# Performance work log

Measured on AMD Instinct MI355X. Metric: run time of the kernel, lower is better.

Reference implementation:

```python
import jax, jax.numpy as jnp
import numpy as np

BN_EPS = 1e-5


def setup_inputs() -> dict:
    key = jax.random.key(0)
    ks = jax.random.split(key, 6)
    B, C, H, W = 4, 256, 64, 64
    Ci = 128
    s_in = 0.02  # small init scale for conv weights
    x = jax.random.normal(ks[0], (B, C, H, W), dtype=jnp.float32)
    g_w = jax.random.normal(ks[1], (Ci, C), dtype=jnp.float32) * s_in
    theta_w = jax.random.normal(ks[2], (Ci, C), dtype=jnp.float32) * s_in
    phi_w = jax.random.normal(ks[3], (Ci, C), dtype=jnp.float32) * s_in
    W_w = jax.random.normal(ks[4], (C, Ci), dtype=jnp.float32) * s_in
    return {
        "x": x,
        "g_w": g_w, "g_b": jnp.zeros((Ci,), jnp.float32),
        "theta_w": theta_w, "theta_b": jnp.zeros((Ci,), jnp.float32),
        "phi_w": phi_w, "phi_b": jnp.zeros((Ci,), jnp.float32),
        "W_w": W_w, "W_b": jnp.zeros((C,), jnp.float32),
        "bn_gamma": jnp.ones((C,), jnp.float32),
        "bn_beta": jnp.zeros((C,), jnp.float32),
    }


def reference(x, g_w, g_b, theta_w, theta_b, phi_w, phi_b, W_w, W_b, bn_gamma, bn_beta):
    B, C, H, W = x.shape
    N = H * W
    xf = x.reshape(B, C, N)  # flatten spatial -> [B, C, N]

    def conv1x1(w, b):  # 1x1 conv == per-position linear over channels
        return jnp.einsum('oc,bcn->bon', w, xf) + b[None, :, None]

    g_x = conv1x1(g_w, g_b)          # [B, Ci, N]
    theta_x = conv1x1(theta_w, theta_b)
    phi_x = conv1x1(phi_w, phi_b)

    f = jnp.einsum('bcn,bcm->bnm', theta_x, phi_x)   # [B, N, N] attention logits
    attn = jax.nn.softmax(f, axis=-1)
    y = jnp.einsum('bnm,bcm->bcn', attn, g_x)        # [B, Ci, N]

    Wy = jnp.einsum('oc,bcn->bon', W_w, y) + W_b[None, :, None]  # [B, C, N]
    Wy = Wy.reshape(B, C, H, W)

    # BatchNorm2d in training mode (default): batch statistics over (B, H, W)
    mean = Wy.mean(axis=(0, 2, 3))
    var = Wy.var(axis=(0, 2, 3))
    Wy_bn = (bn_gamma[None, :, None, None] * (Wy - mean[None, :, None, None])
             * jax.lax.rsqrt(var[None, :, None, None] + BN_EPS)
             + bn_beta[None, :, None, None])
    return Wy_bn + x
```

## Files before the change

kernel.cpp:

```cpp
#include <hip/hip_runtime.h>
#include <hip/hip_bf16.h>

typedef __attribute__((ext_vector_type(8))) __bf16 bf16x8;
typedef __attribute__((ext_vector_type(4))) __bf16 bf16x4;
typedef __attribute__((ext_vector_type(4))) float  f32x4;
typedef __attribute__((ext_vector_type(16))) float f32x16;

#define L2E 1.44269504088896340736f

static __device__ __forceinline__ f32x4 mfma16(bf16x8 a, bf16x8 b, f32x4 c) {
    return __builtin_amdgcn_mfma_f32_16x16x32_bf16(a, b, c, 0, 0, 0);
}
static __device__ __forceinline__ f32x16 mfma32(bf16x8 a, bf16x8 b, f32x16 c) {
    return __builtin_amdgcn_mfma_f32_32x32x16_bf16(a, b, c, 0, 0, 0);
}

#define GLOAD_LDS16(gsrc, ldst)                                                \
    __builtin_amdgcn_global_load_lds(                                          \
        (const __attribute__((address_space(1))) unsigned int*)(gsrc),         \
        (__attribute__((address_space(3))) unsigned int*)(ldst), 16, 0, 0)

__global__ __launch_bounds__(256) void prep_w(
    const float* __restrict__ thw, const float* __restrict__ phw,
    const float* __restrict__ gw,  const float* __restrict__ Ww,
    __bf16* __restrict__ wbf)
{
    const int idx  = blockIdx.x * 256 + threadIdx.x;
    const int base = idx * 4;
    const float* src = (base < 32768) ? thw : (base < 65536) ? phw
                     : (base < 98304) ? gw  : Ww;
    const int off = base & 32767;
    f32x4 v = *reinterpret_cast<const f32x4*>(src + off);
    bf16x4 o;
    #pragma unroll
    for (int i = 0; i < 4; ++i) o[i] = (__bf16)v[i];
    *reinterpret_cast<bf16x4*>(wbf + base) = o;
}

__global__ __launch_bounds__(256) void xT_kernel(
    const float* __restrict__ x, __bf16* __restrict__ xT)
{
    __shared__ float tile[64][65];
    const int b  = blockIdx.z;
    const int c0 = blockIdx.y * 64;
    const int n0 = blockIdx.x * 64;
    const int tr = threadIdx.x >> 4;
    const int tc = threadIdx.x & 15;
    #pragma unroll
    for (int k = 0; k < 4; ++k) {
        int c = k * 16 + tr;
        f32x4 v = *reinterpret_cast<const f32x4*>(
            x + ((size_t)b * 256 + c0 + c) * 4096 + n0 + tc * 4);
        #pragma unroll
        for (int i = 0; i < 4; ++i) tile[c][tc * 4 + i] = v[i];
    }
    __syncthreads();
    #pragma unroll
    for (int k = 0; k < 4; ++k) {
        int n = k * 16 + tr;
        bf16x4 v;
        #pragma unroll
        for (int i = 0; i < 4; ++i) v[i] = (__bf16)tile[tc * 4 + i][n];
        *reinterpret_cast<bf16x4*>(xT + ((size_t)b * 4096 + n0 + n) * 256 + c0 + tc * 4) = v;
    }
}

__global__ __launch_bounds__(256, 1) void proj_mfma(
    const __bf16* __restrict__ xT, const __bf16* __restrict__ wbf,
    const float* __restrict__ bth, const float* __restrict__ bph,
    const float* __restrict__ bg,
    __bf16* __restrict__ thetaT, __bf16* __restrict__ phiT, __bf16* __restrict__ gT)
{
    const int p    = blockIdx.y;
    const int b    = blockIdx.z;
    const int n0   = blockIdx.x * 64;
    const int w    = threadIdx.x >> 6;
    const int lane = threadIdx.x & 63;
    const int lo   = lane & 15;
    const int hi   = lane >> 4;

    __shared__ alignas(16) __bf16 XA[64 * 256];
    __shared__ alignas(16) __bf16 WL[128 * 256];

    const __bf16* wsrc  = wbf + p * 32768;
    const float*  bias  = (p == 0) ? bth : (p == 1) ? bph : bg;
    __bf16*       out   = (p == 0) ? thetaT : (p == 1) ? phiT : gT;
    const __bf16* xbase = xT + ((size_t)b * 4096 + n0) * 256;

    #pragma unroll
    for (int u = 0; u < 8; ++u) {
        const int chunk = (w * 8 + u) * 64 + lane;
        const int row   = chunk >> 5;
        const int jb    = (chunk & 31) * 16;
        const int sb    = row * 512 + (jb ^ ((row & 7) << 4));
        GLOAD_LDS16(xbase + (sb >> 1), &XA[(w * 8 + u) * 512]);
    }
    #pragma unroll
    for (int u = 0; u < 16; ++u) {
        const int chunk = (w * 16 + u) * 64 + lane;
        const int row   = chunk >> 5;
        const int jb    = (chunk & 31) * 16;
        const int sb    = row * 512 + (jb ^ ((row & 7) << 4));
        GLOAD_LDS16(wsrc + (sb >> 1), &WL[(w * 16 + u) * 512]);
    }
    __syncthreads();

    f32x4 C[8];
    #pragma unroll
    for (int cc = 0; cc < 8; ++cc) C[cc] = f32x4{0.f, 0.f, 0.f, 0.f};

    const int arow = w * 16 + lo;
    #pragma unroll
    for (int kb = 0; kb < 8; ++kb) {
        const int koff = kb * 64 + hi * 16;
        bf16x8 a = *reinterpret_cast<const bf16x8*>(
            (const char*)XA + arow * 512 + (koff ^ ((arow & 7) << 4)));
        bf16x8 bb[8];
        #pragma unroll
        for (int cc = 0; cc < 8; ++cc) {
            const int o = cc * 16 + lo;
            bb[cc] = *reinterpret_cast<const bf16x8*>(
                (const char*)WL + o * 512 + (koff ^ ((o & 7) << 4)));
        }
        #pragma unroll
        for (int cc = 0; cc < 8; ++cc) C[cc] = mfma16(a, bb[cc], C[cc]);
    }

    const int nbase = n0 + w * 16;
    #pragma unroll
    for (int cc = 0; cc < 8; ++cc) {
        const float bv = bias[cc * 16 + lo];
        #pragma unroll
        for (int r = 0; r < 4; ++r)
            out[((size_t)b * 4096 + nbase + 4 * hi + r) * 128 + cc * 16 + lo] =
                (__bf16)(C[cc][r] + bv);
    }
}

__global__ __launch_bounds__(256) void transpose_g(
    const __bf16* __restrict__ gT, __bf16* __restrict__ gBlk)
{
    __shared__ __bf16 tile[64][66];
    const int b  = blockIdx.z;
    const int c0 = blockIdx.y * 64;
    const int n0 = blockIdx.x * 64;
    const int tr = threadIdx.x >> 4;
    const int tc = threadIdx.x & 15;
    #pragma unroll
    for (int k = 0; k < 4; ++k) {
        int row = k * 16 + tr;
        bf16x4 v = *reinterpret_cast<const bf16x4*>(
            gT + ((size_t)b * 4096 + n0 + row) * 128 + c0 + tc * 4);
        #pragma unroll
        for (int i = 0; i < 4; ++i) tile[row][tc * 4 + i] = v[i];
    }
    __syncthreads();
    #pragma unroll
    for (int k = 0; k < 4; ++k) {
        int c = k * 16 + tr;
        int n = n0 + tc * 4;
        int mt = n >> 5, mm = n & 31;
        int g  = mm >> 2;
        int gp = (g & 4) | ((g & 1) << 1) | ((g >> 1) & 1);
        int mmP = (gp << 2) | (mm & 3);
        bf16x4 v;
        #pragma unroll
        for (int i = 0; i < 4; ++i) v[i] = tile[tc * 4 + i][c];
        *reinterpret_cast<bf16x4*>(
            gBlk + (((size_t)(b * 128 + mt) * 128) + (c0 + c)) * 32 + mmP) = v;
    }
}

template<int NCH>
__global__ __launch_bounds__(256, 3) void attn_kernel(
    const __bf16* __restrict__ thetaT, const __bf16* __restrict__ phiT,
    const __bf16* __restrict__ gBlk, __bf16* __restrict__ yPart,
    float* __restrict__ lPart)
{
    constexpr int SH = (NCH == 8) ? 3 : 2;
    constexpr int NT = (4096 / NCH) / 32;
    const int bid   = blockIdx.x;
    const int chunk = bid & (NCH - 1);
    const int qb    = (bid >> SH) & 31;
    const int b     = bid >> (SH + 5);
    const int w     = threadIdx.x >> 6;
    const int lane  = threadIdx.x & 63;
    const int l31   = lane & 31;
    const int h2    = lane >> 5;
    const int Q0    = qb * 128 + w * 32;
    const int kvbase = chunk * (4096 / NCH);

    __shared__ alignas(16) __bf16 Kt[3][32 * 128];
    __shared__ alignas(16) __bf16 Vt[3][128 * 32];

    bf16x8 qf[8];
    {
        const __bf16* qrow = thetaT + ((size_t)b * 4096 + Q0 + l31) * 128 + h2 * 8;
        #pragma unroll
        for (int ks = 0; ks < 8; ++ks)
            qf[ks] = *reinterpret_cast<const bf16x8*>(qrow + ks * 16);
    }

    f32x16 yacc[4];
    #pragma unroll
    for (int ct = 0; ct < 4; ++ct)
        #pragma unroll
        for (int r = 0; r < 16; ++r) yacc[ct][r] = 0.f;
    float ylrun = 0.f;

    const __bf16* phiB   = phiT + (size_t)b * 4096 * 128;
    const __bf16* gBlk_b = gBlk + (size_t)b * 128 * 4096;

    auto stage = [&](int buf, int t) {
        const int kv = kvbase + t * 32;
        #pragma unroll
        for (int u = 0; u < 2; ++u) {
            const int ii   = w + u * 4;
            const int mrow = ii * 4 + (lane >> 4);
            const int cbl  = ((lane & 15) * 16) ^ ((mrow & 7) << 4);
            const __bf16* src = phiB + ((size_t)(kv + mrow) << 7) + (cbl >> 1);
            GLOAD_LDS16(src, &Kt[buf][ii * 512]);
        }
        const __bf16* vtile = gBlk_b + ((size_t)(kv >> 5) << 12);
        #pragma unroll
        for (int u = 0; u < 2; ++u) {
            const int jj = w + u * 4;
            const int ch = jj * 64 + lane;
            const int c  = ch >> 2;
            const int h  = (ch & 3) ^ ((c >> 1) & 3);
            const __bf16* src = vtile + c * 32 + h * 8;
            GLOAD_LDS16(src, &Vt[buf][jj * 512]);
        }
    };

    stage(0, 0);
    stage(1, 1);

    int ia = 0, ib = 1, ic = 2;
    const int sw = (l31 >> 1) & 3;

    #pragma unroll 1
    for (int t = 0; t < NT; ++t) {
        if (t < NT - 2) {
            stage(ic, t + 2);
            asm volatile("s_waitcnt vmcnt(8)" ::: "memory");
        } else if (t == NT - 2) {
            asm volatile("s_waitcnt vmcnt(4)" ::: "memory");
        } else {
            asm volatile("s_waitcnt vmcnt(0)" ::: "memory");
        }
        __builtin_amdgcn_s_barrier();
        __builtin_amdgcn_sched_barrier(0);

        const char* Kb = (const char*)&Kt[ia][0];
        const char* Vb = (const char*)&Vt[ia][0];

        f32x16 S;
        #pragma unroll
        for (int r = 0; r < 16; ++r) S[r] = 0.f;
        #pragma unroll
        for (int ks = 0; ks < 8; ++ks) {
            bf16x8 ka = *reinterpret_cast<const bf16x8*>(
                Kb + l31 * 256 + ((ks * 32 + h2 * 16) ^ ((l31 & 7) << 4)));
            S = mfma32(ka, qf[ks], S);
        }

        float p[16];
        #pragma unroll
        for (int r = 0; r < 16; ++r) p[r] = __builtin_amdgcn_exp2f(S[r] * L2E);
        float ls = 0.f;
        #pragma unroll
        for (int r = 0; r < 16; ++r) ls += p[r];
        ylrun += ls;
        bf16x8 pa0, pa1;
        #pragma unroll
        for (int e = 0; e < 8; ++e) { pa0[e] = (__bf16)p[e]; pa1[e] = (__bf16)p[8 + e]; }

        #pragma unroll
        for (int ct = 0; ct < 4; ++ct) {
            const int vrow = (ct * 32 + l31) * 64;
            bf16x8 v0 = *reinterpret_cast<const bf16x8*>(
                Vb + vrow + ((h2 ^ sw) << 4));
            bf16x8 v1 = *reinterpret_cast<const bf16x8*>(
                Vb + vrow + (((2 + h2) ^ sw) << 4));
            yacc[ct] = mfma32(pa0, v0, yacc[ct]);
            yacc[ct] = mfma32(pa1, v1, yacc[ct]);
        }

        asm volatile("" ::: "memory");
        __builtin_amdgcn_s_barrier();
        __builtin_amdgcn_sched_barrier(0);
        const int tmp = ia; ia = ib; ib = ic; ic = tmp;
    }

    const float ylt = ylrun + __shfl_xor(ylrun, 32);
    const int bc = chunk * 4 + b;
    #pragma unroll
    for (int ct = 0; ct < 4; ++ct)
        #pragma unroll
        for (int r = 0; r < 16; ++r) {
            const int q = Q0 + (r & 3) + 8 * (r >> 2) + 4 * h2;
            yPart[((size_t)bc * 4096 + q) * 128 + ct * 32 + l31] = (__bf16)yacc[ct][r];
        }
    if (h2 == 0)
        lPart[(size_t)bc * 4096 + Q0 + l31] = ylt;
}

template<int NC>
__global__ __launch_bounds__(256) void merge_kernel(
    const __bf16* __restrict__ yPart, const float* __restrict__ lPart,
    __bf16* __restrict__ yT)
{
    const int idx = blockIdx.x * 256 + threadIdx.x;
    const int row = idx >> 5;
    const int c4  = (idx & 31) * 4;
    float lsum = 0.f;
    #pragma unroll
    for (int c = 0; c < NC; ++c) lsum += lPart[(size_t)c * 16384 + row];
    const float inv = 1.0f / lsum;
    float s[4] = {0.f, 0.f, 0.f, 0.f};
    #pragma unroll
    for (int c = 0; c < NC; ++c) {
        bf16x4 v = *reinterpret_cast<const bf16x4*>(
            yPart + (size_t)c * 2097152 + (size_t)row * 128 + c4);
        #pragma unroll
        for (int i = 0; i < 4; ++i) s[i] += (float)v[i];
    }
    bf16x4 o;
    #pragma unroll
    for (int i = 0; i < 4; ++i) o[i] = (__bf16)(s[i] * inv);
    *reinterpret_cast<bf16x4*>(yT + (size_t)row * 128 + c4) = o;
}

__global__ __launch_bounds__(256, 1) void wy_mfma(
    const __bf16* __restrict__ yT, const __bf16* __restrict__ wW,
    const float* __restrict__ Wb, float* __restrict__ Wy, float* __restrict__ pSQ)
{
    const int b    = blockIdx.y;
    const int n0   = blockIdx.x * 128;
    const int w    = threadIdx.x >> 6;
    const int lane = threadIdx.x & 63;
    const int lo   = lane & 15;
    const int hi   = lane >> 4;

    __shared__ alignas(16) __bf16 YL[128 * 128];
    __shared__ alignas(16) __bf16 WL[256 * 128];

    const __bf16* ybase = yT + ((size_t)b * 4096 + n0) * 128;
    #pragma unroll
    for (int u = 0; u < 8; ++u) {
        const int chunk = (w * 8 + u) * 64 + lane;
        const int row   = chunk >> 4;
        const int jb    = (chunk & 15) * 16;
        const int sb    = row * 256 + (jb ^ ((row & 7) << 4));
        GLOAD_LDS16(ybase + (sb >> 1), &YL[(w * 8 + u) * 512]);
    }
    #pragma unroll
    for (int u = 0; u < 16; ++u) {
        const int chunk = (w * 16 + u) * 64 + lane;
        const int row   = chunk >> 4;
        const int jb    = (chunk & 15) * 16;
        const int sb    = row * 256 + (jb ^ ((row & 7) << 4));
        GLOAD_LDS16(wW + (sb >> 1), &WL[(w * 16 + u) * 512]);
    }
    __syncthreads();

    f32x4 C[4][8];
    #pragma unroll
    for (int og = 0; og < 4; ++og)
        #pragma unroll
        for (int ct = 0; ct < 8; ++ct) C[og][ct] = f32x4{0.f, 0.f, 0.f, 0.f};

    #pragma unroll
    for (int kb = 0; kb < 4; ++kb) {
        const int koff = kb * 64 + hi * 16;
        bf16x8 a[4], bb[8];
        #pragma unroll
        for (int og = 0; og < 4; ++og) {
            const int o = w * 64 + og * 16 + lo;
            a[og] = *reinterpret_cast<const bf16x8*>(
                (const char*)WL + o * 256 + (koff ^ ((o & 7) << 4)));
        }
        #pragma unroll
        for (int ct = 0; ct < 8; ++ct) {
            const int nl = ct * 16 + lo;
            bb[ct] = *reinterpret_cast<const bf16x8*>(
                (const char*)YL + nl * 256 + (koff ^ ((nl & 7) << 4)));
        }
        #pragma unroll
        for (int og = 0; og < 4; ++og)
            #pragma unroll
            for (int ct = 0; ct < 8; ++ct)
                C[og][ct] = mfma16(a[og], bb[ct], C[og][ct]);
    }

    const int blk = blockIdx.y * 32 + blockIdx.x;
    #pragma unroll
    for (int og = 0; og < 4; ++og)
        #pragma unroll
        for (int r = 0; r < 4; ++r) {
            const int o  = w * 64 + og * 16 + 4 * hi + r;
            const float bv = Wb[o];
            float s = 0.f, q = 0.f;
            #pragma unroll
            for (int ct = 0; ct < 8; ++ct) {
                const float v = C[og][ct][r] + bv;
                Wy[((size_t)b * 256 + o) * 4096 + n0 + ct * 16 + lo] = v;
                s += v; q += v * v;
            }
            #pragma unroll
            for (int off = 1; off <= 8; off <<= 1) {
                s += __shfl_xor(s, off);
                q += __shfl_xor(q, off);
            }
            if (lo == 0) {
                pSQ[blk * 256 + o]         = s;
                pSQ[32768 + blk * 256 + o] = q;
            }
        }
}

__global__ __launch_bounds__(128) void stats_finalize(
    const float* __restrict__ pSQ, const float* __restrict__ gamma,
    const float* __restrict__ beta, float* __restrict__ stats)
{
    const int o = blockIdx.x;
    const int t = threadIdx.x;
    float s = pSQ[t * 256 + o];
    float q = pSQ[32768 + t * 256 + o];
    #pragma unroll
    for (int off = 32; off >= 1; off >>= 1) {
        s += __shfl_down(s, off);
        q += __shfl_down(q, off);
    }
    __shared__ float red[4];
    if ((t & 63) == 0) { red[t >> 6] = s; red[2 + (t >> 6)] = q; }
    __syncthreads();
    if (t == 0) {
        const float S = red[0] + red[1];
        const float Q = red[2] + red[3];
        const float mean = S * (1.f / 16384.f);
        const float var  = Q * (1.f / 16384.f) - mean * mean;
        const float scl  = gamma[o] * rsqrtf(var + 1e-5f);
        stats[o]       = scl;
        stats[256 + o] = beta[o] - mean * scl;
    }
}

__global__ __launch_bounds__(256) void final_kernel(
    const float* __restrict__ Wy, const float* __restrict__ x,
    const float* __restrict__ stats, float* __restrict__ out)
{
    const int idx = blockIdx.x * 256 + threadIdx.x;
    const int o   = (idx >> 10) & 255;
    f32x4 wy = *reinterpret_cast<const f32x4*>(Wy + (size_t)idx * 4);
    f32x4 xv = *reinterpret_cast<const f32x4*>(x  + (size_t)idx * 4);
    f32x4 res = wy * stats[o] + stats[256 + o] + xv;
    *reinterpret_cast<f32x4*>(out + (size_t)idx * 4) = res;
}

extern "C" void kernel_launch(void* const* d_in, const int* in_sizes, int n_in,
                              void* d_out, int out_size, void* d_ws, size_t ws_size,
                              hipStream_t stream)
{
    const float* x    = (const float*)d_in[0];
    const float* g_w  = (const float*)d_in[1];
    const float* g_b  = (const float*)d_in[2];
    const float* th_w = (const float*)d_in[3];
    const float* th_b = (const float*)d_in[4];
    const float* ph_w = (const float*)d_in[5];
    const float* ph_b = (const float*)d_in[6];
    const float* W_w  = (const float*)d_in[7];
    const float* W_b  = (const float*)d_in[8];
    const float* bn_g = (const float*)d_in[9];
    const float* bn_b = (const float*)d_in[10];
    float* out = (float*)d_out;

    char* ws = (char*)d_ws;
    const size_t MB = 1u << 20;
    __bf16* thetaT = (__bf16*)(ws);
    __bf16* phiT   = (__bf16*)(ws + 4 * MB);
    __bf16* gBlk   = (__bf16*)(ws + 8 * MB);
    __bf16* gT     = (__bf16*)(ws + 12 * MB);
    __bf16* xT     = (__bf16*)(ws + 16 * MB);
    __bf16* yPart  = (__bf16*)(ws + 12 * MB);
    __bf16* yT     = (__bf16*)(ws);
    float*  Wy     = (float*) (ws + 4 * MB);
    float*  pSQ    = (float*) (ws + 20 * MB);

    const bool big = ws_size >= 46926848ull;
    const size_t tail = big ? 44 * MB : 28 * MB;
    float*  lPart = (float*) (ws + tail);
    __bf16* wbf   = (__bf16*)(ws + tail + (big ? 524288 : 262144));
    float*  stats = (float*) (ws + tail + (big ? 786432 : 524288));

    prep_w<<<dim3(128), 256, 0, stream>>>(th_w, ph_w, g_w, W_w, wbf);
    xT_kernel<<<dim3(64, 4, 4), 256, 0, stream>>>(x, xT);
    proj_mfma<<<dim3(64, 3, 4), 256, 0, stream>>>(
        xT, wbf, th_b, ph_b, g_b, thetaT, phiT, gT);
    transpose_g<<<dim3(64, 2, 4), 256, 0, stream>>>(gT, gBlk);
    if (big) {
        attn_kernel<8><<<dim3(1024), 256, 0, stream>>>(thetaT, phiT, gBlk, yPart, lPart);
        merge_kernel<8><<<dim3(2048), 256, 0, stream>>>(yPart, lPart, yT);
    } else {
        attn_kernel<4><<<dim3(512), 256, 0, stream>>>(thetaT, phiT, gBlk, yPart, lPart);
        merge_kernel<4><<<dim3(2048), 256, 0, stream>>>(yPart, lPart, yT);
    }
    wy_mfma<<<dim3(32, 4), 256, 0, stream>>>(yT, wbf + 98304, W_b, Wy, pSQ);
    stats_finalize<<<dim3(256), 128, 0, stream>>>(pSQ, bn_g, bn_b, stats);
    final_kernel<<<dim3(4096), 256, 0, stream>>>(Wy, x, stats, out);
}
```

Baseline: 102.1 us.

## Process two query tiles per wave in attention kernel with 2-wave blocks

Each wave now handles 64 query rows as two 32-row tiles and reuses every K and V fragment read from LDS for both tiles. The block shrinks from four waves to two, and each wave issues twice as many global-to-LDS loads per stage, with the vmcnt waits raised to match. The aim is to halve LDS read traffic per MFMA and raise arithmetic intensity. In exchange, per-wave register pressure roughly doubles (two sets of accumulators, Q fragments and S tiles), which may cut occupancy or cause spills, and there are fewer waves per block to hide latency.

Result: slower. 122.6 us (+20.1%).

```diff
diff --git a/kernel.cpp b/kernel.cpp
--- a/kernel.cpp
+++ b/kernel.cpp
@@ -172,7 +172,7 @@
 }
 
 template<int NCH>
-__global__ __launch_bounds__(256, 3) void attn_kernel(
+__global__ __launch_bounds__(128) void attn_kernel(
     const __bf16* __restrict__ thetaT, const __bf16* __restrict__ phiT,
     const __bf16* __restrict__ gBlk, __bf16* __restrict__ yPart,
     float* __restrict__ lPart)
@@ -187,26 +187,29 @@
     const int lane  = threadIdx.x & 63;
     const int l31   = lane & 31;
     const int h2    = lane >> 5;
-    const int Q0    = qb * 128 + w * 32;
+    const int Q0    = qb * 128 + w * 64;
     const int kvbase = chunk * (4096 / NCH);
 
     __shared__ alignas(16) __bf16 Kt[3][32 * 128];
     __shared__ alignas(16) __bf16 Vt[3][128 * 32];
 
-    bf16x8 qf[8];
-    {
-        const __bf16* qrow = thetaT + ((size_t)b * 4096 + Q0 + l31) * 128 + h2 * 8;
+    bf16x8 qf[2][8];
+    #pragma unroll
+    for (int j = 0; j < 2; ++j) {
+        const __bf16* qrow = thetaT + ((size_t)b * 4096 + Q0 + j * 32 + l31) * 128 + h2 * 8;
         #pragma unroll
         for (int ks = 0; ks < 8; ++ks)
-            qf[ks] = *reinterpret_cast<const bf16x8*>(qrow + ks * 16);
-    }
-
-    f32x16 yacc[4];
-    #pragma unroll
-    for (int ct = 0; ct < 4; ++ct)
-        #pragma unroll
-        for (int r = 0; r < 16; ++r) yacc[ct][r] = 0.f;
-    float ylrun = 0.f;
+            qf[j][ks] = *reinterpret_cast<const bf16x8*>(qrow + ks * 16);
+    }
+
+    f32x16 yacc[2][4];
+    #pragma unroll
+    for (int j = 0; j < 2; ++j)
+        #pragma unroll
+        for (int ct = 0; ct < 4; ++ct)
+            #pragma unroll
+            for (int r = 0; r < 16; ++r) yacc[j][ct][r] = 0.f;
+    float ylrun0 = 0.f, ylrun1 = 0.f;
 
     const __bf16* phiB   = phiT + (size_t)b * 4096 * 128;
     const __bf16* gBlk_b = gBlk + (size_t)b * 128 * 4096;
@@ -214,22 +217,22 @@
     auto stage = [&](int buf, int t) {
         const int kv = kvbase + t * 32;
         #pragma unroll
-        for (int u = 0; u < 2; ++u) {
-            const int ii   = w + u * 4;
-            const int mrow = ii * 4 + (lane >> 4);
-            const int cbl  = ((lane & 15) * 16) ^ ((mrow & 7) << 4);
-            const __bf16* src = phiB + ((size_t)(kv + mrow) << 7) + (cbl >> 1);
-            GLOAD_LDS16(src, &Kt[buf][ii * 512]);
+        for (int u = 0; u < 4; ++u) {
+            const int ck   = (w * 4 + u) * 64 + lane;
+            const int mrow = ck >> 4;
+            const int jb   = (ck & 15) << 4;
+            const __bf16* src = phiB + ((size_t)(kv + mrow) << 7)
+                              + ((jb ^ ((mrow & 7) << 4)) >> 1);
+            GLOAD_LDS16(src, &Kt[buf][(w * 4 + u) * 512]);
         }
         const __bf16* vtile = gBlk_b + ((size_t)(kv >> 5) << 12);
         #pragma unroll
-        for (int u = 0; u < 2; ++u) {
-            const int jj = w + u * 4;
-            const int ch = jj * 64 + lane;
-            const int c  = ch >> 2;
-            const int h  = (ch & 3) ^ ((c >> 1) & 3);
+        for (int u = 0; u < 4; ++u) {
+            const int ck = (w * 4 + u) * 64 + lane;
+            const int c  = ck >> 2;
+            const int h  = (ck & 3) ^ ((c >> 1) & 3);
             const __bf16* src = vtile + c * 32 + h * 8;
-            GLOAD_LDS16(src, &Vt[buf][jj * 512]);
+            GLOAD_LDS16(src, &Vt[buf][(w * 4 + u) * 512]);
         }
     };
 
@@ -243,9 +246,9 @@
     for (int t = 0; t < NT; ++t) {
         if (t < NT - 2) {
             stage(ic, t + 2);
+            asm volatile("s_waitcnt vmcnt(16)" ::: "memory");
+        } else if (t == NT - 2) {
             asm volatile("s_waitcnt vmcnt(8)" ::: "memory");
-        } else if (t == NT - 2) {
-            asm volatile("s_waitcnt vmcnt(4)" ::: "memory");
         } else {
             asm volatile("s_waitcnt vmcnt(0)" ::: "memory");
         }
@@ -255,36 +258,44 @@
         const char* Kb = (const char*)&Kt[ia][0];
         const char* Vb = (const char*)&Vt[ia][0];
 
-        f32x16 S;
-        #pragma unroll
-        for (int r = 0; r < 16; ++r) S[r] = 0.f;
+        f32x16 S0, S1;
+        #pragma unroll
+        for (int r = 0; r < 16; ++r) { S0[r] = 0.f; S1[r] = 0.f; }
         #pragma unroll
         for (int ks = 0; ks < 8; ++ks) {
             bf16x8 ka = *reinterpret_cast<const bf16x8*>(
                 Kb + l31 * 256 + ((ks * 32 + h2 * 16) ^ ((l31 & 7) << 4)));
-            S = mfma32(ka, qf[ks], S);
-        }
-
-        float p[16];
-        #pragma unroll
-        for (int r = 0; r < 16; ++r) p[r] = __builtin_amdgcn_exp2f(S[r] * L2E);
-        float ls = 0.f;
-        #pragma unroll
-        for (int r = 0; r < 16; ++r) ls += p[r];
-        ylrun += ls;
-        bf16x8 pa0, pa1;
-        #pragma unroll
-        for (int e = 0; e < 8; ++e) { pa0[e] = (__bf16)p[e]; pa1[e] = (__bf16)p[8 + e]; }
+            S0 = mfma32(ka, qf[0][ks], S0);
+            S1 = mfma32(ka, qf[1][ks], S1);
+        }
+
+        bf16x8 pa[2][2];
+        {
+            float p0[16], p1[16];
+            float ls0 = 0.f, ls1 = 0.f;
+            #pragma unroll
+            for (int r = 0; r < 16; ++r) {
+                p0[r] = __builtin_amdgcn_exp2f(S0[r] * L2E);
+                p1[r] = __builtin_amdgcn_exp2f(S1[r] * L2E);
+                ls0 += p0[r]; ls1 += p1[r];
+            }
+            ylrun0 += ls0; ylrun1 += ls1;
+            #pragma unroll
+            for (int e = 0; e < 8; ++e) {
+                pa[0][0][e] = (__bf16)p0[e]; pa[0][1][e] = (__bf16)p0[8 + e];
+                pa[1][0][e] = (__bf16)p1[e]; pa[1][1][e] = (__bf16)p1[8 + e];
+            }
+        }
 
         #pragma unroll
         for (int ct = 0; ct < 4; ++ct) {
             const int vrow = (ct * 32 + l31) * 64;
-            bf16x8 v0 = *reinterpret_cast<const bf16x8*>(
-                Vb + vrow + ((h2 ^ sw) << 4));
-            bf16x8 v1 = *reinterpret_cast<const bf16x8*>(
-                Vb + vrow + (((2 + h2) ^ sw) << 4));
-            yacc[ct] = mfma32(pa0, v0, yacc[ct]);
-            yacc[ct] = mfma32(pa1, v1, yacc[ct]);
+            bf16x8 v0 = *reinterpret_cast<const bf16x8*>(Vb + vrow + ((h2 ^ sw) << 4));
+            bf16x8 v1 = *reinterpret_cast<const bf16x8*>(Vb + vrow + (((2 + h2) ^ sw) << 4));
+            yacc[0][ct] = mfma32(pa[0][0], v0, yacc[0][ct]);
+            yacc[0][ct] = mfma32(pa[0][1], v1, yacc[0][ct]);
+            yacc[1][ct] = mfma32(pa[1][0], v0, yacc[1][ct]);
+            yacc[1][ct] = mfma32(pa[1][1], v1, yacc[1][ct]);
         }
 
         asm volatile("" ::: "memory");
@@ -293,17 +304,23 @@
         const int tmp = ia; ia = ib; ib = ic; ic = tmp;
     }
 
-    const float ylt = ylrun + __shfl_xor(ylrun, 32);
+    const float ylt0 = ylrun0 + __shfl_xor(ylrun0, 32);
+    const float ylt1 = ylrun1 + __shfl_xor(ylrun1, 32);
     const int bc = chunk * 4 + b;
     #pragma unroll
-    for (int ct = 0; ct < 4; ++ct)
-        #pragma unroll
-        for (int r = 0; r < 16; ++r) {
-            const int q = Q0 + (r & 3) + 8 * (r >> 2) + 4 * h2;
-            yPart[((size_t)bc * 4096 + q) * 128 + ct * 32 + l31] = (__bf16)yacc[ct][r];
-        }
-    if (h2 == 0)
-        lPart[(size_t)bc * 4096 + Q0 + l31] = ylt;
+    for (int j = 0; j < 2; ++j)
+        #pragma unroll
+        for (int ct = 0; ct < 4; ++ct)
+            #pragma unroll
+            for (int r = 0; r < 16; ++r) {
+                const int q = Q0 + j * 32 + (r & 3) + 8 * (r >> 2) + 4 * h2;
+                yPart[((size_t)bc * 4096 + q) * 128 + ct * 32 + l31] =
+                    (__bf16)yacc[j][ct][r];
+            }
+    if (h2 == 0) {
+        lPart[(size_t)bc * 4096 + Q0 + l31]      = ylt0;
+        lPart[(size_t)bc * 4096 + Q0 + 32 + l31] = ylt1;
+    }
 }
 
 template<int NC>
@@ -500,10 +517,10 @@
         xT, wbf, th_b, ph_b, g_b, thetaT, phiT, gT);
     transpose_g<<<dim3(64, 2, 4), 256, 0, stream>>>(gT, gBlk);
     if (big) {
-        attn_kernel<8><<<dim3(1024), 256, 0, stream>>>(thetaT, phiT, gBlk, yPart, lPart);
+        attn_kernel<8><<<dim3(1024), 128, 0, stream>>>(thetaT, phiT, gBlk, yPart, lPart);
         merge_kernel<8><<<dim3(2048), 256, 0, stream>>>(yPart, lPart, yT);
     } else {
-        attn_kernel<4><<<dim3(512), 256, 0, stream>>>(thetaT, phiT, gBlk, yPart, lPart);
+        attn_kernel<4><<<dim3(512), 128, 0, stream>>>(thetaT, phiT, gBlk, yPart, lPart);
         merge_kernel<4><<<dim3(2048), 256, 0, stream>>>(yPart, lPart, yT);
     }
     wy_mfma<<<dim3(32, 4), 256, 0, stream>>>(yT, wbf + 98304, W_b, Wy, pSQ);
```

## Fuse g transpose into projection, merge partials into Wy GEMM, store Wy as bf16

Applied to the files above, without the earlier changes.

The g-branch of the projection kernel now transposes through LDS and writes the blocked gBlk layout directly, which removes the separate transpose_g kernel and its gT round trip. The merge kernel is replaced by a small linv kernel. The Wy GEMM now sums the attention partial outputs while staging them into LDS and applies the softmax normalisation per column after the MFMA. Wy is stored as bf16 instead of fp32 to halve that intermediate's write and read traffic. Trade-offs are halved Wy tiles (more blocks, more partial stats), extra bf16 rounding of Wy before batch-norm, and global partial-sum reads no longer using async LDS loads.

Result: faster. 94.24 us (-7.7%).

```diff
diff --git a/kernel.cpp b/kernel.cpp
--- a/kernel.cpp
+++ b/kernel.cpp
@@ -69,7 +69,7 @@
     const __bf16* __restrict__ xT, const __bf16* __restrict__ wbf,
     const float* __restrict__ bth, const float* __restrict__ bph,
     const float* __restrict__ bg,
-    __bf16* __restrict__ thetaT, __bf16* __restrict__ phiT, __bf16* __restrict__ gT)
+    __bf16* __restrict__ thetaT, __bf16* __restrict__ phiT, __bf16* __restrict__ gBlk)
 {
     const int p    = blockIdx.y;
     const int b    = blockIdx.z;
@@ -84,7 +84,6 @@
 
     const __bf16* wsrc  = wbf + p * 32768;
     const float*  bias  = (p == 0) ? bth : (p == 1) ? bph : bg;
-    __bf16*       out   = (p == 0) ? thetaT : (p == 1) ? phiT : gT;
     const __bf16* xbase = xT + ((size_t)b * 4096 + n0) * 256;
 
     #pragma unroll
@@ -126,48 +125,45 @@
         for (int cc = 0; cc < 8; ++cc) C[cc] = mfma16(a, bb[cc], C[cc]);
     }
 
-    const int nbase = n0 + w * 16;
-    #pragma unroll
-    for (int cc = 0; cc < 8; ++cc) {
-        const float bv = bias[cc * 16 + lo];
-        #pragma unroll
-        for (int r = 0; r < 4; ++r)
-            out[((size_t)b * 4096 + nbase + 4 * hi + r) * 128 + cc * 16 + lo] =
-                (__bf16)(C[cc][r] + bv);
-    }
-}
-
-__global__ __launch_bounds__(256) void transpose_g(
-    const __bf16* __restrict__ gT, __bf16* __restrict__ gBlk)
-{
-    __shared__ __bf16 tile[64][66];
-    const int b  = blockIdx.z;
-    const int c0 = blockIdx.y * 64;
-    const int n0 = blockIdx.x * 64;
-    const int tr = threadIdx.x >> 4;
-    const int tc = threadIdx.x & 15;
-    #pragma unroll
-    for (int k = 0; k < 4; ++k) {
-        int row = k * 16 + tr;
-        bf16x4 v = *reinterpret_cast<const bf16x4*>(
-            gT + ((size_t)b * 4096 + n0 + row) * 128 + c0 + tc * 4);
-        #pragma unroll
-        for (int i = 0; i < 4; ++i) tile[row][tc * 4 + i] = v[i];
-    }
-    __syncthreads();
-    #pragma unroll
-    for (int k = 0; k < 4; ++k) {
-        int c = k * 16 + tr;
-        int n = n0 + tc * 4;
-        int mt = n >> 5, mm = n & 31;
-        int g  = mm >> 2;
-        int gp = (g & 4) | ((g & 1) << 1) | ((g >> 1) & 1);
-        int mmP = (gp << 2) | (mm & 3);
-        bf16x4 v;
-        #pragma unroll
-        for (int i = 0; i < 4; ++i) v[i] = tile[tc * 4 + i][c];
-        *reinterpret_cast<bf16x4*>(
-            gBlk + (((size_t)(b * 128 + mt) * 128) + (c0 + c)) * 32 + mmP) = v;
+    if (p < 2) {
+        __bf16* out = (p == 0) ? thetaT : phiT;
+        const int nbase = n0 + w * 16;
+        #pragma unroll
+        for (int cc = 0; cc < 8; ++cc) {
+            const float bv = bias[cc * 16 + lo];
+            #pragma unroll
+            for (int r = 0; r < 4; ++r)
+                out[((size_t)b * 4096 + nbase + 4 * hi + r) * 128 + cc * 16 + lo] =
+                    (__bf16)(C[cc][r] + bv);
+        }
+    } else {
+        __syncthreads();
+        __bf16* T = &XA[0];
+        const int nl0 = w * 16 + 4 * hi;
+        #pragma unroll
+        for (int cc = 0; cc < 8; ++cc) {
+            const float bv = bias[cc * 16 + lo];
+            #pragma unroll
+            for (int r = 0; r < 4; ++r)
+                T[(cc * 16 + lo) * 66 + nl0 + r] = (__bf16)(C[cc][r] + bv);
+        }
+        __syncthreads();
+        #pragma unroll
+        for (int q8 = 0; q8 < 8; ++q8) {
+            const int qid = q8 * 256 + threadIdx.x;
+            const int c   = qid >> 4;
+            const int nl  = (qid & 15) * 4;
+            const int n   = n0 + nl;
+            const int mt  = n >> 5;
+            const int mm  = n & 31;
+            const int g   = mm >> 2;
+            const int gp  = (g & 4) | ((g & 1) << 1) | ((g >> 1) & 1);
+            bf16x4 v;
+            #pragma unroll
+            for (int i = 0; i < 4; ++i) v[i] = T[c * 66 + nl + i];
+            *reinterpret_cast<bf16x4*>(
+                gBlk + (((size_t)(b * 128 + mt)) * 128 + c) * 32 + (gp << 2)) = v;
+        }
     }
 }
 
@@ -279,10 +275,8 @@
         #pragma unroll
         for (int ct = 0; ct < 4; ++ct) {
             const int vrow = (ct * 32 + l31) * 64;
-            bf16x8 v0 = *reinterpret_cast<const bf16x8*>(
-                Vb + vrow + ((h2 ^ sw) << 4));
-            bf16x8 v1 = *reinterpret_cast<const bf16x8*>(
-                Vb + vrow + (((2 + h2) ^ sw) << 4));
+            bf16x8 v0 = *reinterpret_cast<const bf16x8*>(Vb + vrow + ((h2 ^ sw) << 4));
+            bf16x8 v1 = *reinterpret_cast<const bf16x8*>(Vb + vrow + (((2 + h2) ^ sw) << 4));
             yacc[ct] = mfma32(pa0, v0, yacc[ct]);
             yacc[ct] = mfma32(pa1, v1, yacc[ct]);
         }
@@ -307,54 +301,32 @@
 }
 
 template<int NC>
-__global__ __launch_bounds__(256) void merge_kernel(
-    const __bf16* __restrict__ yPart, const float* __restrict__ lPart,
-    __bf16* __restrict__ yT)
-{
-    const int idx = blockIdx.x * 256 + threadIdx.x;
-    const int row = idx >> 5;
-    const int c4  = (idx & 31) * 4;
-    float lsum = 0.f;
-    #pragma unroll
-    for (int c = 0; c < NC; ++c) lsum += lPart[(size_t)c * 16384 + row];
-    const float inv = 1.0f / lsum;
-    float s[4] = {0.f, 0.f, 0.f, 0.f};
-    #pragma unroll
-    for (int c = 0; c < NC; ++c) {
-        bf16x4 v = *reinterpret_cast<const bf16x4*>(
-            yPart + (size_t)c * 2097152 + (size_t)row * 128 + c4);
-        #pragma unroll
-        for (int i = 0; i < 4; ++i) s[i] += (float)v[i];
-    }
-    bf16x4 o;
-    #pragma unroll
-    for (int i = 0; i < 4; ++i) o[i] = (__bf16)(s[i] * inv);
-    *reinterpret_cast<bf16x4*>(yT + (size_t)row * 128 + c4) = o;
-}
-
+__global__ __launch_bounds__(256) void linv_kernel(
+    const float* __restrict__ lPart, float* __restrict__ linv)
+{
+    const int i = blockIdx.x * 256 + threadIdx.x;
+    float s = 0.f;
+    #pragma unroll
+    for (int c = 0; c < NC; ++c) s += lPart[(size_t)c * 16384 + i];
+    linv[i] = 1.0f / s;
+}
+
+template<int NC>
 __global__ __launch_bounds__(256, 1) void wy_mfma(
-    const __bf16* __restrict__ yT, const __bf16* __restrict__ wW,
-    const float* __restrict__ Wb, float* __restrict__ Wy, float* __restrict__ pSQ)
+    const __bf16* __restrict__ yPart, const float* __restrict__ linv,
+    const __bf16* __restrict__ wW, const float* __restrict__ Wb,
+    __bf16* __restrict__ Wy, float* __restrict__ pSQ)
 {
     const int b    = blockIdx.y;
-    const int n0   = blockIdx.x * 128;
+    const int n0   = blockIdx.x * 64;
     const int w    = threadIdx.x >> 6;
     const int lane = threadIdx.x & 63;
     const int lo   = lane & 15;
     const int hi   = lane >> 4;
 
-    __shared__ alignas(16) __bf16 YL[128 * 128];
+    __shared__ alignas(16) __bf16 YL[64 * 128];
     __shared__ alignas(16) __bf16 WL[256 * 128];
 
-    const __bf16* ybase = yT + ((size_t)b * 4096 + n0) * 128;
-    #pragma unroll
-    for (int u = 0; u < 8; ++u) {
-        const int chunk = (w * 8 + u) * 64 + lane;
-        const int row   = chunk >> 4;
-        const int jb    = (chunk & 15) * 16;
-        const int sb    = row * 256 + (jb ^ ((row & 7) << 4));
-        GLOAD_LDS16(ybase + (sb >> 1), &YL[(w * 8 + u) * 512]);
-    }
     #pragma unroll
     for (int u = 0; u < 16; ++u) {
         const int chunk = (w * 16 + u) * 64 + lane;
@@ -363,18 +335,39 @@
         const int sb    = row * 256 + (jb ^ ((row & 7) << 4));
         GLOAD_LDS16(wW + (sb >> 1), &WL[(w * 16 + u) * 512]);
     }
+    #pragma unroll
+    for (int u = 0; u < 4; ++u) {
+        const int ch   = u * 256 + threadIdx.x;
+        const int row  = ch >> 4;
+        const int col8 = ch & 15;
+        float acc8[8];
+        #pragma unroll
+        for (int e = 0; e < 8; ++e) acc8[e] = 0.f;
+        #pragma unroll
+        for (int c = 0; c < NC; ++c) {
+            bf16x8 v = *reinterpret_cast<const bf16x8*>(
+                yPart + ((size_t)(c * 4 + b) * 4096 + n0 + row) * 128 + col8 * 8);
+            #pragma unroll
+            for (int e = 0; e < 8; ++e) acc8[e] += (float)v[e];
+        }
+        bf16x8 o8;
+        #pragma unroll
+        for (int e = 0; e < 8; ++e) o8[e] = (__bf16)acc8[e];
+        *reinterpret_cast<bf16x8*>(
+            (char*)YL + row * 256 + ((col8 * 16) ^ ((row & 7) << 4))) = o8;
+    }
     __syncthreads();
 
-    f32x4 C[4][8];
+    f32x4 C[4][4];
     #pragma unroll
     for (int og = 0; og < 4; ++og)
         #pragma unroll
-        for (int ct = 0; ct < 8; ++ct) C[og][ct] = f32x4{0.f, 0.f, 0.f, 0.f};
+        for (int ct = 0; ct < 4; ++ct) C[og][ct] = f32x4{0.f, 0.f, 0.f, 0.f};
 
     #pragma unroll
     for (int kb = 0; kb < 4; ++kb) {
         const int koff = kb * 64 + hi * 16;
-        bf16x8 a[4], bb[8];
+        bf16x8 a[4], bb[4];
         #pragma unroll
         for (int og = 0; og < 4; ++og) {
             const int o = w * 64 + og * 16 + lo;
@@ -382,7 +375,7 @@
                 (const char*)WL + o * 256 + (koff ^ ((o & 7) << 4)));
         }
         #pragma unroll
-        for (int ct = 0; ct < 8; ++ct) {
+        for (int ct = 0; ct < 4; ++ct) {
             const int nl = ct * 16 + lo;
             bb[ct] = *reinterpret_cast<const bf16x8*>(
                 (const char*)YL + nl * 256 + (koff ^ ((nl & 7) << 4)));
@@ -390,11 +383,16 @@
         #pragma unroll
         for (int og = 0; og < 4; ++og)
             #pragma unroll
-            for (int ct = 0; ct < 8; ++ct)
+            for (int ct = 0; ct < 4; ++ct)
                 C[og][ct] = mfma16(a[og], bb[ct], C[og][ct]);
     }
 
-    const int blk = blockIdx.y * 32 + blockIdx.x;
+    float linvv[4];
+    #pragma unroll
+    for (int ct = 0; ct < 4; ++ct)
+        linvv[ct] = linv[b * 4096 + n0 + ct * 16 + lo];
+
+    const int blk = blockIdx.y * 64 + blockIdx.x;
     #pragma unroll
     for (int og = 0; og < 4; ++og)
         #pragma unroll
@@ -403,9 +401,9 @@
             const float bv = Wb[o];
             float s = 0.f, q = 0.f;
             #pragma unroll
-            for (int ct = 0; ct < 8; ++ct) {
-                const float v = C[og][ct][r] + bv;
-                Wy[((size_t)b * 256 + o) * 4096 + n0 + ct * 16 + lo] = v;
+            for (int ct = 0; ct < 4; ++ct) {
+                const float v = C[og][ct][r] * linvv[ct] + bv;
+                Wy[((size_t)b * 256 + o) * 4096 + n0 + ct * 16 + lo] = (__bf16)v;
                 s += v; q += v * v;
             }
             #pragma unroll
@@ -415,30 +413,31 @@
             }
             if (lo == 0) {
                 pSQ[blk * 256 + o]         = s;
-                pSQ[32768 + blk * 256 + o] = q;
+                pSQ[65536 + blk * 256 + o] = q;
             }
         }
 }
 
-__global__ __launch_bounds__(128) void stats_finalize(
+__global__ __launch_bounds__(256) void stats_finalize(
     const float* __restrict__ pSQ, const float* __restrict__ gamma,
     const float* __restrict__ beta, float* __restrict__ stats)
 {
     const int o = blockIdx.x;
     const int t = threadIdx.x;
     float s = pSQ[t * 256 + o];
-    float q = pSQ[32768 + t * 256 + o];
+    float q = pSQ[65536 + t * 256 + o];
     #pragma unroll
     for (int off = 32; off >= 1; off >>= 1) {
         s += __shfl_down(s, off);
         q += __shfl_down(q, off);
     }
-    __shared__ float red[4];
-    if ((t & 63) == 0) { red[t >> 6] = s; red[2 + (t >> 6)] = q; }
+    __shared__ float red[8];
+    const int wid = t >> 6;
+    if ((t & 63) == 0) { red[wid] = s; red[4 + wid] = q; }
     __syncthreads();
     if (t == 0) {
-        const float S = red[0] + red[1];
-        const float Q = red[2] + red[3];
+        const float S = red[0] + red[1] + red[2] + red[3];
+        const float Q = red[4] + red[5] + red[6] + red[7];
         const float mean = S * (1.f / 16384.f);
         const float var  = Q * (1.f / 16384.f) - mean * mean;
         const float scl  = gamma[o] * rsqrtf(var + 1e-5f);
@@ -448,14 +447,17 @@
 }
 
 __global__ __launch_bounds__(256) void final_kernel(
-    const float* __restrict__ Wy, const float* __restrict__ x,
+    const __bf16* __restrict__ Wy, const float* __restrict__ x,
     const float* __restrict__ stats, float* __restrict__ out)
 {
     const int idx = blockIdx.x * 256 + threadIdx.x;
     const int o   = (idx >> 10) & 255;
-    f32x4 wy = *reinterpret_cast<const f32x4*>(Wy + (size_t)idx * 4);
-    f32x4 xv = *reinterpret_cast<const f32x4*>(x  + (size_t)idx * 4);
-    f32x4 res = wy * stats[o] + stats[256 + o] + xv;
+    bf16x4 wyb = *reinterpret_cast<const bf16x4*>(Wy + (size_t)idx * 4);
+    f32x4 xv = *reinterpret_cast<const f32x4*>(x + (size_t)idx * 4);
+    const float scl = stats[o], sh = stats[256 + o];
+    f32x4 res;
+    #pragma unroll
+    for (int i = 0; i < 4; ++i) res[i] = (float)wyb[i] * scl + sh + xv[i];
     *reinterpret_cast<f32x4*>(out + (size_t)idx * 4) = res;
 }
 
@@ -481,12 +483,11 @@
     __bf16* thetaT = (__bf16*)(ws);
     __bf16* phiT   = (__bf16*)(ws + 4 * MB);
     __bf16* gBlk   = (__bf16*)(ws + 8 * MB);
-    __bf16* gT     = (__bf16*)(ws + 12 * MB);
-    __bf16* xT     = (__bf16*)(ws + 16 * MB);
+    __bf16* xT     = (__bf16*)(ws + 12 * MB);
     __bf16* yPart  = (__bf16*)(ws + 12 * MB);
-    __bf16* yT     = (__bf16*)(ws);
-    float*  Wy     = (float*) (ws + 4 * MB);
-    float*  pSQ    = (float*) (ws + 20 * MB);
+    __bf16* Wy     = (__bf16*)(ws);
+    float*  pSQ    = (float*) (ws + 8 * MB);
+    float*  linv   = (float*) (ws + 8 * MB + 524288);
 
     const bool big = ws_size >= 46926848ull;
     const size_t tail = big ? 44 * MB : 28 * MB;
@@ -497,16 +498,16 @@
     prep_w<<<dim3(128), 256, 0, stream>>>(th_w, ph_w, g_w, W_w, wbf);
     xT_kernel<<<dim3(64, 4, 4), 256, 0, stream>>>(x, xT);
     proj_mfma<<<dim3(64, 3, 4), 256, 0, stream>>>(
-        xT, wbf, th_b, ph_b, g_b, thetaT, phiT, gT);
-    transpose_g<<<dim3(64, 2, 4), 256, 0, stream>>>(gT, gBlk);
+        xT, wbf, th_b, ph_b, g_b, thetaT, phiT, gBlk);
     if (big) {
         attn_kernel<8><<<dim3(1024), 256, 0, stream>>>(thetaT, phiT, gBlk, yPart, lPart);
-        merge_kernel<8><<<dim3(2048), 256, 0, stream>>>(yPart, lPart, yT);
+        linv_kernel<8><<<dim3(64), 256, 0, stream>>>(lPart, linv);
+        wy_mfma<8><<<dim3(64, 4), 256, 0, stream>>>(yPart, linv, wbf + 98304, W_b, Wy, pSQ);
     } else {
         attn_kernel<4><<<dim3(512), 256, 0, stream>>>(thetaT, phiT, gBlk, yPart, lPart);
-        merge_kernel<4><<<dim3(2048), 256, 0, stream>>>(yPart, lPart, yT);
-    }
-    wy_mfma<<<dim3(32, 4), 256, 0, stream>>>(yT, wbf + 98304, W_b, Wy, pSQ);
-    stats_finalize<<<dim3(256), 128, 0, stream>>>(pSQ, bn_g, bn_b, stats);
+        linv_kernel<4><<<dim3(64), 256, 0, stream>>>(lPart, linv);
+        wy_mfma<4><<<dim3(64, 4), 256, 0, stream>>>(yPart, linv, wbf + 98304, W_b, Wy, pSQ);
+    }
+    stats_finalize<<<dim3(256), 256, 0, stream>>>(pSQ, bn_g, bn_b, stats);
     final_kernel<<<dim3(4096), 256, 0, stream>>>(Wy, x, stats, out);
 }
```
